# Kernel optimization log

Hardware: AMD Instinct MI355X
Metric: run time of the kernel (lower is better)

The kernel has to match this reference:

```python
import jax, jax.numpy as jnp
import numpy as np

NUM_LEVELS = 16
LEVEL_DIM = 2
BASE_RES = 16
MAX_RES = 2048
HASHMAP_SIZE = 1 << 19
N_POINTS = 2000000

# Instant-NGP geometric progression of grid resolutions
_scale = np.exp2(np.log2(MAX_RES / BASE_RES) / (NUM_LEVELS - 1))
RESOLUTIONS = [int(np.ceil(BASE_RES * _scale ** l)) for l in range(NUM_LEVELS)]

# corner offsets of the unit cube, shape [8, 3]
_OFFS = np.stack(np.meshgrid([0, 1], [0, 1], [0, 1], indexing='ij'), -1).reshape(8, 3)
_PRIMES = np.array([1, 2654435761, 805459861], dtype=np.uint32)


def grid_encode(x, table):
    """x: [N,3] in [0,1]; table: [L, T, F] -> [N, L*F]."""
    offs = jnp.asarray(_OFFS, dtype=jnp.int32)          # [8,3]
    feats = []
    for l, res in enumerate(RESOLUTIONS):
        pos = x * (res - 1)                              # [N,3]
        pos_i = jnp.clip(jnp.floor(pos).astype(jnp.int32), 0, res - 2)
        frac = pos - pos_i.astype(pos.dtype)             # [N,3]
        corners = pos_i[:, None, :] + offs[None]         # [N,8,3]
        if res ** 3 <= HASHMAP_SIZE:
            # dense (collision-free) indexing for coarse levels
            idx = corners[..., 0] + res * (corners[..., 1] + res * corners[..., 2])
        else:
            # spatial hash: xor of coordinate * prime, mod table size
            c = corners.astype(jnp.uint32)
            h = (c[..., 0] * _PRIMES[0]) ^ (c[..., 1] * _PRIMES[1]) ^ (c[..., 2] * _PRIMES[2])
            idx = (h % jnp.uint32(HASHMAP_SIZE)).astype(jnp.int32)
        vals = table[l][idx]                             # [N,8,F] gather
        # multilinear interpolation weights per corner
        w = jnp.prod(jnp.where(offs[None].astype(bool), frac[:, None, :], 1.0 - frac[:, None, :]), axis=-1)  # [N,8]
        feats.append(jnp.einsum('nc,ncf->nf', w, vals))
    return jnp.concatenate(feats, axis=-1)               # [N, 32]


def setup_inputs() -> dict:
    key = jax.random.key(0)
    ks = jax.random.split(key, 6)
    x = jax.random.uniform(ks[0], (N_POINTS, 3), dtype=jnp.float32)
    table = jax.random.uniform(ks[1], (NUM_LEVELS, HASHMAP_SIZE, LEVEL_DIM),
                               dtype=jnp.float32, minval=-1e-4, maxval=1e-4)
    in_dim = NUM_LEVELS * LEVEL_DIM  # 32
    W1 = jax.random.normal(ks[2], (in_dim, 64), dtype=jnp.float32) / np.sqrt(in_dim)
    W2 = jax.random.normal(ks[3], (64, 64), dtype=jnp.float32) / 8.0
    W3 = jax.random.normal(ks[4], (64, 64), dtype=jnp.float32) / 8.0
    Wo = jax.random.normal(ks[5], (64, 1), dtype=jnp.float32) / 8.0
    z = lambda n: jnp.zeros((n,), dtype=jnp.float32)
    return {"x": x, "table": table, "W1": W1, "b1": z(64), "W2": W2, "b2": z(64),
            "W3": W3, "b3": z(64), "Wo": Wo, "bo": z(1)}


def reference(x, table, W1, b1, W2, b2, W3, b3, Wo, bo):
    h = grid_encode(x, table)                 # [N,32]
    h = jax.nn.relu(h @ W1 + b1)
    h = jax.nn.relu(h @ W2 + b2)
    h = jax.nn.relu(h @ W3 + b3)
    return h @ Wo + bo                        # [N,1]
```

## Files before the change

### kernel.cpp

```cpp
#include <hip/hip_runtime.h>
#include <hip/hip_fp16.h>
#include <cmath>
#include <cstdint>


#define HASH_SZ (1u << 19)
#define HMASK   (HASH_SZ - 1u)
#define PR2 2654435761u
#define PR3 805459861u

typedef float v2f __attribute__((ext_vector_type(2)));
typedef float v4f __attribute__((ext_vector_type(4)));
typedef v4f v4fu __attribute__((aligned(8)));
typedef v2f v2fu __attribute__((aligned(8)));
typedef short bf16x8 __attribute__((ext_vector_type(8)));
typedef float f32x4 __attribute__((ext_vector_type(4)));
typedef unsigned int u32;
typedef u32 u32x2 __attribute__((ext_vector_type(2)));
typedef u32 u32x4 __attribute__((ext_vector_type(4)));
typedef u32x4 u32x4u __attribute__((aligned(8)));

struct ResArr { int r[16]; };

__device__ __forceinline__ unsigned short bf16_rne(float f) {
    union { float f; unsigned u; } v; v.f = f;
    unsigned u = v.u;
    unsigned r = (u + 0x7fffu + ((u >> 16) & 1u)) >> 16;
    return (unsigned short)r;
}
__device__ __forceinline__ float bf16f(unsigned short h) {
    union { unsigned u; float f; } v; v.u = ((unsigned)h) << 16;
    return v.f;
}
__device__ __forceinline__ void split8(const float* x, bf16x8& hi, bf16x8& lo) {
    #pragma unroll
    for (int j = 0; j < 8; ++j) {
        union { float f; unsigned u; } v; v.f = x[j];
        const unsigned hu = v.u & 0xffff0000u;
        hi[j] = (short)(hu >> 16);
        union { unsigned u; float f; } hf; hf.u = hu;
        const float d = x[j] - hf.f;
        union { float f; unsigned u; } dv; dv.f = d;
        lo[j] = (short)((dv.u + 0x7fffu + ((dv.u >> 16) & 1u)) >> 16);
    }
}
__device__ __forceinline__ u32 rne16u(float f) {
    union { float f; u32 u; } v; v.f = f;
    return (v.u + 0x7fffu + ((v.u >> 16) & 1u)) >> 16;
}
__device__ __forceinline__ u32x2 pack_split2(float f0, float f1) {
    union { float f; u32 u; } a, b; a.f = f0; b.f = f1;
    const u32 h0 = a.u & 0xffff0000u, h1 = b.u & 0xffff0000u;
    union { u32 u; float f; } ha, hb; ha.u = h0; hb.u = h1;
    u32x2 r;
    r.x = (h0 >> 16) | h1;
    r.y = rne16u(f0 - ha.f) | (rne16u(f1 - hb.f) << 16);
    return r;
}

__device__ __forceinline__ u32 pkh(float f0, float f1) {
    const __half h0 = __float2half_rn(f0), h1 = __float2half_rn(f1);
    return (u32)__half_as_ushort(h0) | ((u32)__half_as_ushort(h1) << 16);
}
__device__ __forceinline__ v2f cvt2(u32 e) {
    __half2 h;
    *reinterpret_cast<u32*>(&h) = e;
    v2f r; r.x = __low2float(h); r.y = __high2float(h);
    return r;
}
__device__ __forceinline__ u32 sel4(u32x4 P, u32 k) {
    const u32 a = (k & 1u) ? P.y : P.x;
    const u32 b = (k & 1u) ? P.w : P.z;
    return (k & 2u) ? b : a;
}

__global__ __launch_bounds__(256, 8)
void cvt_table(const float* __restrict__ table, u32* __restrict__ tab16, int total)
{
    const int e0 = (blockIdx.x * 256 + threadIdx.x) * 4;
    if (e0 >= total) return;
    const v4f a = __builtin_nontemporal_load((const v4f*)(table + 2 * (size_t)e0));
    const v4f b = __builtin_nontemporal_load((const v4f*)(table + 2 * (size_t)e0 + 4));
    u32x4 o;
    o.x = pkh(a.x, a.y); o.y = pkh(a.z, a.w);
    o.z = pkh(b.x, b.y); o.w = pkh(b.z, b.w);
    *(u32x4*)(tab16 + e0) = o;
}

__device__ __forceinline__ void gather16_one(
    const u32* __restrict__ tab, int res, bool dense,
    float px, float py, float pz, float& A0, float& A1)
{
    const float rf = (float)(res - 1);
    const float fx = px * rf, fy = py * rf, fz = pz * rf;
    int ix = (int)floorf(fx), iy = (int)floorf(fy), iz = (int)floorf(fz);
    ix = min(max(ix, 0), res - 2);
    iy = min(max(iy, 0), res - 2);
    iz = min(max(iz, 0), res - 2);
    const float tx = fx - (float)ix, ty = fy - (float)iy, tz = fz - (float)iz;
    const float sx = 1.f - tx, sy = 1.f - ty, sz = 1.f - tz;
    float a0 = 0.f, a1 = 0.f;

    if (dense) {
        const int b0 = ix + res * (iy + res * iz);
        #pragma unroll
        for (int c = 0; c < 4; ++c) {
            const int dy = c >> 1, dz = c & 1;
            const u32 idx0 = (u32)(b0 + res * dy + res * res * dz);
            const u32x4u Pv = *(const u32x4u*)(tab + (idx0 & ~1u));
            const bool hi = (idx0 & 1u) != 0u;
            const u32 e0 = hi ? Pv.y : Pv.x;
            const u32 e1 = hi ? Pv.z : Pv.y;
            const float wyz = (dy ? ty : sy) * (dz ? tz : sz);
            const float w0 = sx * wyz, w1 = tx * wyz;
            const v2f f0 = cvt2(e0), f1 = cvt2(e1);
            a0 = fmaf(w0, f0.x, a0); a1 = fmaf(w0, f0.y, a1);
            a0 = fmaf(w1, f1.x, a0); a1 = fmaf(w1, f1.y, a1);
        }
    } else {
        u32 i1a[4], k0[4];
        u32x4 P[4];
        #pragma unroll
        for (int c = 0; c < 4; ++c) {
            const int dy = c >> 1, dz = c & 1;
            const u32 r = (u32)(iy + dy) * PR2 ^ (u32)(iz + dz) * PR3;
            const u32 i0 = ((u32)ix ^ r) & HMASK;
            i1a[c] = ((u32)(ix + 1) ^ r) & HMASK;
            k0[c] = i0 & 3u;
            P[c] = *(const u32x4*)(tab + (i0 & ~3u));
        }
        const bool extra = ((ix & 3) == 3);
        u32 O[4];
        if (extra) {
            #pragma unroll
            for (int c = 0; c < 4; ++c) O[c] = tab[i1a[c]];
        } else {
            #pragma unroll
            for (int c = 0; c < 4; ++c) O[c] = 0u;
        }
        #pragma unroll
        for (int c = 0; c < 4; ++c) {
            const int dy = c >> 1, dz = c & 1;
            const u32 e0 = sel4(P[c], k0[c]);
            const u32 e1w = sel4(P[c], i1a[c] & 3u);
            const u32 e1 = extra ? O[c] : e1w;
            const float wyz = (dy ? ty : sy) * (dz ? tz : sz);
            const float w0 = sx * wyz, w1 = tx * wyz;
            const v2f f0 = cvt2(e0), f1 = cvt2(e1);
            a0 = fmaf(w0, f0.x, a0); a1 = fmaf(w0, f0.y, a1);
            a0 = fmaf(w1, f1.x, a0); a1 = fmaf(w1, f1.y, a1);
        }
    }
    A0 = a0; A1 = a1;
}

__global__ void prep_weights(const float* __restrict__ W1,
                             const float* __restrict__ W2,
                             const float* __restrict__ W3,
                             unsigned short* __restrict__ wb)
{
    const int tid = threadIdx.x;
    const int nb = tid >> 6, lane = tid & 63;
    const int l15 = lane & 15, q = lane >> 4;
    #pragma unroll
    for (int j = 0; j < 8; ++j) {
        const float v = W1[(q * 8 + j) * 64 + nb * 16 + l15];
        const unsigned short h = bf16_rne(v);
        wb[(nb * 64 + lane) * 8 + j] = h;
        wb[2048 + (nb * 64 + lane) * 8 + j] = bf16_rne(v - bf16f(h));
    }
    #pragma unroll
    for (int kb = 0; kb < 2; ++kb) {
        #pragma unroll
        for (int j = 0; j < 8; ++j) {
            const int row = kb * 32 + q * 8 + j;
            const int idx = ((kb * 4 + nb) * 64 + lane) * 8 + j;
            float v = W2[row * 64 + nb * 16 + l15];
            unsigned short h = bf16_rne(v);
            wb[4096 + idx] = h;
            wb[8192 + idx] = bf16_rne(v - bf16f(h));
            v = W3[row * 64 + nb * 16 + l15];
            h = bf16_rne(v);
            wb[12288 + idx] = h;
            wb[16384 + idx] = bf16_rne(v - bf16f(h));
        }
    }
}

__device__ __forceinline__ void mlp_block(
    const u32x2* __restrict__ featT,
    const unsigned short* __restrict__ wb,
    const float* __restrict__ b1, const float* __restrict__ b2,
    const float* __restrict__ b3,
    const float* __restrict__ Wo, const float* __restrict__ bo,
    float* __restrict__ out, int n, int ns, int mb)
{
    const int wave = threadIdx.x >> 6;
    const int lane = threadIdx.x & 63;
    const int l15 = lane & 15, quad = lane >> 4;
    const int p0 = (mb * 4 + wave) * 32;
    if (p0 >= n) return;

    bf16x8 bh[2], bl[2];
    #pragma unroll
    for (int t = 0; t < 2; ++t) {
        const int p = p0 + t * 16 + l15;
        const int pl = (p < n) ? p : (n - 1);
        u32x4 hw, lw;
        #pragma unroll
        for (int jj = 0; jj < 4; ++jj) {
            const u32x2 v = featT[(size_t)(quad * 4 + jj) * ns + pl];
            hw[jj] = v.x; lw[jj] = v.y;
        }
        bh[t] = *(bf16x8*)&hw;
        bl[t] = *(bf16x8*)&lw;
    }

    f32x4 acc[2][4];
    #pragma unroll
    for (int nb = 0; nb < 4; ++nb) {
        const bf16x8 wh = *(const bf16x8*)(wb + (nb * 64 + lane) * 8);
        const bf16x8 wl = *(const bf16x8*)(wb + 2048 + (nb * 64 + lane) * 8);
        const f32x4 bv = *(const f32x4*)(b1 + nb * 16 + quad * 4);
        #pragma unroll
        for (int t = 0; t < 2; ++t) {
            f32x4 c = bv;
            c = __builtin_amdgcn_mfma_f32_16x16x32_bf16(wh, bl[t], c, 0, 0, 0);
            c = __builtin_amdgcn_mfma_f32_16x16x32_bf16(wl, bh[t], c, 0, 0, 0);
            c = __builtin_amdgcn_mfma_f32_16x16x32_bf16(wh, bh[t], c, 0, 0, 0);
            acc[t][nb] = c;
        }
    }

    #pragma unroll
    for (int layer = 0; layer < 2; ++layer) {
        bf16x8 nh[2][2], nl[2][2];
        #pragma unroll
        for (int t = 0; t < 2; ++t) {
            #pragma unroll
            for (int kb = 0; kb < 2; ++kb) {
                float v[8];
                #pragma unroll
                for (int rr = 0; rr < 4; ++rr) {
                    float xq = fmaxf(acc[t][2 * kb][rr],     0.f);
                    float yq = fmaxf(acc[t][2 * kb + 1][rr], 0.f);
                    asm("v_permlane32_swap_b32 %0, %1" : "+v"(xq), "+v"(yq));
                    asm("v_permlane16_swap_b32 %0, %1" : "+v"(xq), "+v"(yq));
                    v[rr]     = xq;
                    v[4 + rr] = yq;
                }
                split8(v, nh[t][kb], nl[t][kb]);
            }
        }
        const int base_h = layer ? 12288 : 4096;
        const int base_l = layer ? 16384 : 8192;
        const float* __restrict__ bias = layer ? b3 : b2;
        #pragma unroll
        for (int nb = 0; nb < 4; ++nb) {
            const f32x4 bv = *(const f32x4*)(bias + nb * 16 + quad * 4);
            f32x4 c[2];
            #pragma unroll
            for (int t = 0; t < 2; ++t) c[t] = bv;
            #pragma unroll
            for (int kb = 0; kb < 2; ++kb) {
                const int idx = ((kb * 4 + nb) * 64 + lane) * 8;
                const bf16x8 wh = *(const bf16x8*)(wb + base_h + idx);
                const bf16x8 wl = *(const bf16x8*)(wb + base_l + idx);
                #pragma unroll
                for (int t = 0; t < 2; ++t) {
                    c[t] = __builtin_amdgcn_mfma_f32_16x16x32_bf16(wh, nl[t][kb], c[t], 0, 0, 0);
                    c[t] = __builtin_amdgcn_mfma_f32_16x16x32_bf16(wl, nh[t][kb], c[t], 0, 0, 0);
                    c[t] = __builtin_amdgcn_mfma_f32_16x16x32_bf16(wh, nh[t][kb], c[t], 0, 0, 0);
                }
            }
            #pragma unroll
            for (int t = 0; t < 2; ++t) acc[t][nb] = c[t];
        }
    }

    float part[2];
    #pragma unroll
    for (int t = 0; t < 2; ++t) {
        float s = 0.f;
        #pragma unroll
        for (int nb = 0; nb < 4; ++nb) {
            const f32x4 wo4 = *(const f32x4*)(Wo + nb * 16 + quad * 4);
            #pragma unroll
            for (int r = 0; r < 4; ++r)
                s = fmaf(fmaxf(acc[t][nb][r], 0.f), wo4[r], s);
        }
        part[t] = s;
    }
    #pragma unroll
    for (int t = 0; t < 2; ++t) {
        part[t] += __shfl_xor(part[t], 16, 64);
        part[t] += __shfl_xor(part[t], 32, 64);
    }
    if (quad == 0) {
        const float b = bo[0];
        #pragma unroll
        for (int t = 0; t < 2; ++t) {
            const int po = p0 + t * 16 + l15;
            if (po < n) out[po] = part[t] + b;
        }
    }
}

__global__ __launch_bounds__(256, 4)
void mlp_mfma(const u32x2* __restrict__ featT,
              const unsigned short* __restrict__ wb,
              const float* __restrict__ b1, const float* __restrict__ b2,
              const float* __restrict__ b3,
              const float* __restrict__ Wo, const float* __restrict__ bo,
              float* __restrict__ out, int n, int ns)
{
    mlp_block(featT, wb, b1, b2, b3, Wo, bo, out, n, ns, blockIdx.x);
}

__global__ __launch_bounds__(256, 4)
void fused_q(const float* __restrict__ xe, const u32* __restrict__ tab16,
             u32x2* __restrict__ fe, int ne, int nse,
             const u32x2* __restrict__ fm,
             const unsigned short* __restrict__ wb,
             const float* __restrict__ b1, const float* __restrict__ b2,
             const float* __restrict__ b3,
             const float* __restrict__ Wo, const float* __restrict__ bo,
             float* __restrict__ outm, int nm, int nsm,
             ResArr rv, int de, int bpl, int M, int ilv)
{
    const int b = blockIdx.x;
    int eb;
    if (ilv) {
        const int q4 = b >> 2, r4 = b & 3;
        if (r4 == 3 && q4 < M) {
            mlp_block(fm, wb, b1, b2, b3, Wo, bo, outm, nm, nsm, q4);
            return;
        }
        eb = b - ((r4 == 3) ? M : min(q4, M));
    } else {
        if (b < M) {
            mlp_block(fm, wb, b1, b2, b3, Wo, bo, outm, nm, nsm, b);
            return;
        }
        eb = b - M;
    }
    const int lvl = eb / bpl;
    if (lvl >= 16) return;
    const int lblk = eb - lvl * bpl;
    const int res = rv.r[lvl];
    const bool dense = (lvl < de);
    const u32* tbl = tab16 + (size_t)lvl * HASH_SZ;

    const int nth2 = bpl * 512;
    for (int q = (lblk * 256 + (int)threadIdx.x) * 2; q < ne; q += nth2) {
        float p0x, p0y, p0z, p1x, p1y, p1z;
        const bool two = (q + 1 < ne);
        if (two) {
            const v4fu a = __builtin_nontemporal_load((const v4fu*)(xe + 3 * q));
            const v2f  bb = __builtin_nontemporal_load((const v2fu*)(xe + 3 * q + 4));
            p0x = a.x; p0y = a.y; p0z = a.z; p1x = a.w; p1y = bb.x; p1z = bb.y;
        } else {
            p0x = xe[3 * q]; p0y = xe[3 * q + 1]; p0z = xe[3 * q + 2];
            p1x = p0x; p1y = p0y; p1z = p0z;
        }
        float a00, a01, a10, a11;
        gather16_one(tbl, res, dense, p0x, p0y, p0z, a00, a01);
        gather16_one(tbl, res, dense, p1x, p1y, p1z, a10, a11);
        if (two) {
            const u32x2 e0 = pack_split2(a00, a01);
            const u32x2 e1 = pack_split2(a10, a11);
            u32x4 st; st.x = e0.x; st.y = e0.y; st.z = e1.x; st.w = e1.y;
            __builtin_nontemporal_store(st, (u32x4*)&fe[(size_t)lvl * nse + q]);
        } else {
            __builtin_nontemporal_store(pack_split2(a00, a01),
                                        &fe[(size_t)lvl * nse + q]);
        }
    }
}

__device__ __forceinline__ void gather_one(
    const v2f* __restrict__ tbl, int res, bool dense,
    float px, float py, float pz, float& A0, float& A1)
{
    const float rf = (float)(res - 1);
    const float fx = px * rf, fy = py * rf, fz = pz * rf;
    int ix = (int)floorf(fx), iy = (int)floorf(fy), iz = (int)floorf(fz);
    ix = min(max(ix, 0), res - 2);
    iy = min(max(iy, 0), res - 2);
    iz = min(max(iz, 0), res - 2);
    const float tx = fx - (float)ix, ty = fy - (float)iy, tz = fz - (float)iz;
    const float sx = 1.f - tx, sy = 1.f - ty, sz = 1.f - tz;
    float a0 = 0.f, a1 = 0.f;

    if (dense) {
        const int b0 = ix + res * (iy + res * iz);
        v4fu P[4];
        #pragma unroll
        for (int c = 0; c < 4; ++c) {
            const int dy = c >> 1, dz = c & 1;
            P[c] = *(const v4fu*)((const float*)tbl + 2 * (b0 + res * dy + res * res * dz));
        }
        #pragma unroll
        for (int c = 0; c < 4; ++c) {
            const int dy = c >> 1, dz = c & 1;
            const float wyz = (dy ? ty : sy) * (dz ? tz : sz);
            const float w0 = sx * wyz, w1 = tx * wyz;
            a0 = fmaf(w0, P[c].x, a0); a1 = fmaf(w0, P[c].y, a1);
            a0 = fmaf(w1, P[c].z, a0); a1 = fmaf(w1, P[c].w, a1);
        }
    } else {
        uint32_t i0[4], i1[4];
        v4f P[4];
        #pragma unroll
        for (int c = 0; c < 4; ++c) {
            const int dy = c >> 1, dz = c & 1;
            const uint32_t r = (uint32_t)(iy + dy) * PR2 ^ (uint32_t)(iz + dz) * PR3;
            i0[c] = ((uint32_t)ix ^ r) & HMASK;
            i1[c] = ((uint32_t)(ix + 1) ^ r) & HMASK;
            P[c] = *(const v4f*)((const float*)tbl + 2 * (i0[c] & ~1u));
        }
        const bool odd = (ix & 1);
        v2f O[4];
        if (odd) {
            #pragma unroll
            for (int c = 0; c < 4; ++c) O[c] = tbl[i1[c]];
        } else {
            #pragma unroll
            for (int c = 0; c < 4; ++c) { v2f z = {0.f, 0.f}; O[c] = z; }
        }
        #pragma unroll
        for (int c = 0; c < 4; ++c) {
            const int dy = c >> 1, dz = c & 1;
            const bool hi = (i0[c] & 1);
            v2f c0, e;
            c0.x = hi ? P[c].z : P[c].x;  c0.y = hi ? P[c].w : P[c].y;
            e.x  = hi ? P[c].x : P[c].z;  e.y  = hi ? P[c].y : P[c].w;
            const v2f c1 = odd ? O[c] : e;
            const float wyz = (dy ? ty : sy) * (dz ? tz : sz);
            const float w0 = sx * wyz, w1 = tx * wyz;
            a0 = fmaf(w0, c0.x, a0); a1 = fmaf(w0, c0.y, a1);
            a0 = fmaf(w1, c1.x, a0); a1 = fmaf(w1, c1.y, a1);
        }
    }
    A0 = a0; A1 = a1;
}

template<int NLEV>
__global__ __launch_bounds__(256, 8)
void encode_k(const float* __restrict__ x, const float* __restrict__ table,
              u32x2* __restrict__ featT, int n, int lb, ResArr rv)
{
    const int nth2 = gridDim.x * 512;
    for (int q = (blockIdx.x * 256 + threadIdx.x) * 2; q < n; q += nth2) {
        float p0x, p0y, p0z, p1x, p1y, p1z;
        const bool two = (q + 1 < n);
        if (two) {
            const v4fu a = __builtin_nontemporal_load((const v4fu*)(x + 3 * q));
            const v2f  b = __builtin_nontemporal_load((const v2fu*)(x + 3 * q + 4));
            p0x = a.x; p0y = a.y; p0z = a.z; p1x = a.w; p1y = b.x; p1z = b.y;
        } else {
            p0x = x[3 * q]; p0y = x[3 * q + 1]; p0z = x[3 * q + 2];
            p1x = p0x; p1y = p0y; p1z = p0z;
        }
        #pragma unroll
        for (int il = 0; il < NLEV; ++il) {
            const int l = lb + il;
            const int res = rv.r[l];
            const bool dense = ((long long)res * res * res <= (long long)HASH_SZ);
            const v2f* tbl = (const v2f*)table + (size_t)l * HASH_SZ;
            float a00, a01, a10, a11;
            gather_one(tbl, res, dense, p0x, p0y, p0z, a00, a01);
            gather_one(tbl, res, dense, p1x, p1y, p1z, a10, a11);
            if (two) {
                const u32x2 e0 = pack_split2(a00, a01);
                const u32x2 e1 = pack_split2(a10, a11);
                u32x4 st; st.x = e0.x; st.y = e0.y; st.z = e1.x; st.w = e1.y;
                __builtin_nontemporal_store(st, (u32x4*)&featT[(size_t)l * n + q]);
            } else {
                __builtin_nontemporal_store(pack_split2(a00, a01),
                                            &featT[(size_t)l * n + q]);
            }
        }
    }
}

__global__ __launch_bounds__(256, 3)
void mlp_forward(const u32x2* __restrict__ featT,
                 const float* __restrict__ W1, const float* __restrict__ b1,
                 const float* __restrict__ W2, const float* __restrict__ b2,
                 const float* __restrict__ W3, const float* __restrict__ b3,
                 const float* __restrict__ Wo, const float* __restrict__ bo,
                 float* __restrict__ out, int n)
{
    const int p = blockIdx.x * 256 + threadIdx.x;
    if (p >= n) return;
    const v2f z2 = {0.f, 0.f};
    v2f A[32], B[32];
    #pragma unroll
    for (int jq = 0; jq < 16; ++jq) {
        const v4f b = *(const v4f*)(b1 + 4 * jq);
        A[2 * jq] = b.xy; A[2 * jq + 1] = b.zw;
    }
    #pragma unroll
    for (int l = 0; l < 16; ++l) {
        const u32x2 e = __builtin_nontemporal_load(&featT[(size_t)l * n + p]);
        union { u32 u; float f; } h0, h1, l0, l1;
        h0.u = e.x << 16; h1.u = e.x & 0xffff0000u;
        l0.u = e.y << 16; l1.u = e.y & 0xffff0000u;
        v2f f; f.x = h0.f + l0.f; f.y = h1.f + l1.f;
        const v4f* w0 = (const v4f*)(W1 + (size_t)(2 * l) * 64);
        const v4f* w1 = (const v4f*)(W1 + (size_t)(2 * l + 1) * 64);
        const v2f hh0 = {f.x, f.x}, hh1 = {f.y, f.y};
        #pragma unroll
        for (int jq = 0; jq < 16; ++jq) {
            const v4f wa = w0[jq];
            A[2 * jq]     = __builtin_elementwise_fma(hh0, wa.xy, A[2 * jq]);
            A[2 * jq + 1] = __builtin_elementwise_fma(hh0, wa.zw, A[2 * jq + 1]);
        }
        #pragma unroll
        for (int jq = 0; jq < 16; ++jq) {
            const v4f wb2 = w1[jq];
            A[2 * jq]     = __builtin_elementwise_fma(hh1, wb2.xy, A[2 * jq]);
            A[2 * jq + 1] = __builtin_elementwise_fma(hh1, wb2.zw, A[2 * jq + 1]);
        }
    }
    #pragma unroll
    for (int j = 0; j < 32; ++j) A[j] = __builtin_elementwise_max(A[j], z2);
    #pragma unroll
    for (int jq = 0; jq < 16; ++jq) {
        const v4f b = *(const v4f*)(b2 + 4 * jq);
        B[2 * jq] = b.xy; B[2 * jq + 1] = b.zw;
    }
    #pragma unroll
    for (int k = 0; k < 64; ++k) {
        const float hv = A[k >> 1][k & 1];
        const v2f h = {hv, hv};
        const v4f* w = (const v4f*)(W2 + (size_t)k * 64);
        #pragma unroll
        for (int jq = 0; jq < 16; ++jq) {
            const v4f wa = w[jq];
            B[2 * jq]     = __builtin_elementwise_fma(h, wa.xy, B[2 * jq]);
            B[2 * jq + 1] = __builtin_elementwise_fma(h, wa.zw, B[2 * jq + 1]);
        }
    }
    #pragma unroll
    for (int j = 0; j < 32; ++j) B[j] = __builtin_elementwise_max(B[j], z2);
    #pragma unroll
    for (int jq = 0; jq < 16; ++jq) {
        const v4f b = *(const v4f*)(b3 + 4 * jq);
        A[2 * jq] = b.xy; A[2 * jq + 1] = b.zw;
    }
    #pragma unroll
    for (int k = 0; k < 64; ++k) {
        const float hv = B[k >> 1][k & 1];
        const v2f h = {hv, hv};
        const v4f* w = (const v4f*)(W3 + (size_t)k * 64);
        #pragma unroll
        for (int jq = 0; jq < 16; ++jq) {
            const v4f wa = w[jq];
            A[2 * jq]     = __builtin_elementwise_fma(h, wa.xy, A[2 * jq]);
            A[2 * jq + 1] = __builtin_elementwise_fma(h, wa.zw, A[2 * jq + 1]);
        }
    }
    v2f o2 = z2;
    #pragma unroll
    for (int jq = 0; jq < 16; ++jq) {
        const v4f wa = *(const v4f*)(Wo + 4 * jq);
        o2 = __builtin_elementwise_fma(__builtin_elementwise_max(A[2 * jq], z2),     wa.xy, o2);
        o2 = __builtin_elementwise_fma(__builtin_elementwise_max(A[2 * jq + 1], z2), wa.zw, o2);
    }
    out[p] = o2.x + o2.y + bo[0];
}

__global__ __launch_bounds__(256, 2)
void hashpinn_fused(const float* __restrict__ x,
                    const float* __restrict__ table,
                    const float* __restrict__ W1, const float* __restrict__ b1,
                    const float* __restrict__ W2, const float* __restrict__ b2,
                    const float* __restrict__ W3, const float* __restrict__ b3,
                    const float* __restrict__ Wo, const float* __restrict__ bo,
                    float* __restrict__ out, int n, ResArr rv)
{
    const int p = blockIdx.x * 256 + threadIdx.x;
    if (p >= n) return;
    const float px = x[3*p+0], py = x[3*p+1], pz = x[3*p+2];
    float feat[32];
    #pragma unroll
    for (int l = 0; l < 16; ++l) {
        const int res = rv.r[l];
        const float rf = (float)(res - 1);
        const float fx = px*rf, fy = py*rf, fz = pz*rf;
        int ix=(int)floorf(fx), iy=(int)floorf(fy), iz=(int)floorf(fz);
        ix=min(max(ix,0),res-2); iy=min(max(iy,0),res-2); iz=min(max(iz,0),res-2);
        const float tx=fx-(float)ix, ty=fy-(float)iy, tz=fz-(float)iz;
        const float sx=1.f-tx, sy=1.f-ty, sz=1.f-tz;
        const float2* tbl=(const float2*)table+(size_t)l*HASH_SZ;
        const bool dense=((long long)res*res*res<=(long long)HASH_SZ);
        float a0=0.f, a1=0.f;
        #pragma unroll
        for (int c=0;c<8;++c){
            const uint32_t cx=(uint32_t)(ix+((c>>2)&1));
            const uint32_t cy=(uint32_t)(iy+((c>>1)&1));
            const uint32_t cz=(uint32_t)(iz+(c&1));
            uint32_t idx = dense ? cx+(uint32_t)res*(cy+(uint32_t)res*cz)
                                 : ((cx*1u ^ cy*PR2 ^ cz*PR3)&HMASK);
            const float2 v=tbl[idx];
            const float w=(((c>>2)&1)?tx:sx)*(((c>>1)&1)?ty:sy)*((c&1)?tz:sz);
            a0=fmaf(w,v.x,a0); a1=fmaf(w,v.y,a1);
        }
        feat[2*l]=a0; feat[2*l+1]=a1;
    }
    float A[64], B[64];
    #pragma unroll
    for (int j=0;j<64;++j) A[j]=b1[j];
    #pragma unroll
    for (int k=0;k<32;++k){ const float h=feat[k];
        #pragma unroll
        for (int j=0;j<64;++j) A[j]=fmaf(h,W1[k*64+j],A[j]); }
    #pragma unroll 1
    for (int it=0;it<2;++it){
        const float* W = it?W3:W2; const float* bb = it?b3:b2;
        #pragma unroll
        for (int j=0;j<64;++j){ A[j]=fmaxf(A[j],0.f); B[j]=bb[j]; }
        #pragma unroll
        for (int k=0;k<64;++k){ const float h=A[k];
            #pragma unroll
            for (int j=0;j<64;++j) B[j]=fmaf(h,W[k*64+j],B[j]); }
        #pragma unroll
        for (int j=0;j<64;++j) A[j]=B[j];
    }
    float o=bo[0];
    #pragma unroll
    for (int j=0;j<64;++j) o=fmaf(fmaxf(A[j],0.f),Wo[j],o);
    out[p]=o;
}

static inline void launch_encode(int nlev, const float* x, const float* table,
                                 u32x2* featT, int n, int lb, const ResArr& rv,
                                 hipStream_t stream) {
    const dim3 g(4096), b(256);
    switch (nlev) {
        case 1: hipLaunchKernelGGL(encode_k<1>, g, b, 0, stream, x, table, featT, n, lb, rv); break;
        case 2: hipLaunchKernelGGL(encode_k<2>, g, b, 0, stream, x, table, featT, n, lb, rv); break;
        case 3: hipLaunchKernelGGL(encode_k<3>, g, b, 0, stream, x, table, featT, n, lb, rv); break;
        case 4: hipLaunchKernelGGL(encode_k<4>, g, b, 0, stream, x, table, featT, n, lb, rv); break;
        case 5: hipLaunchKernelGGL(encode_k<5>, g, b, 0, stream, x, table, featT, n, lb, rv); break;
        case 6: hipLaunchKernelGGL(encode_k<6>, g, b, 0, stream, x, table, featT, n, lb, rv); break;
        case 7: hipLaunchKernelGGL(encode_k<7>, g, b, 0, stream, x, table, featT, n, lb, rv); break;
        default: hipLaunchKernelGGL(encode_k<8>, g, b, 0, stream, x, table, featT, n, lb, rv); break;
    }
}

extern "C" void kernel_launch(void* const* d_in, const int* in_sizes, int n_in,
                              void* d_out, int out_size, void* d_ws, size_t ws_size,
                              hipStream_t stream) {
    const float* x     = (const float*)d_in[0];
    const float* table = (const float*)d_in[1];
    const float* W1    = (const float*)d_in[2];
    const float* b1    = (const float*)d_in[3];
    const float* W2    = (const float*)d_in[4];
    const float* b2    = (const float*)d_in[5];
    const float* W3    = (const float*)d_in[6];
    const float* b3    = (const float*)d_in[7];
    const float* Wo    = (const float*)d_in[8];
    const float* bo    = (const float*)d_in[9];
    float* out = (float*)d_out;

    const int n = in_sizes[0] / 3;

    ResArr rv;
    const double scale = std::exp2(std::log2(2048.0 / 16.0) / 15.0);
    for (int l = 0; l < 16; ++l)
        rv.r[l] = (int)std::ceil(16.0 * std::pow(scale, (double)l));

    int dense_end = 0;
    while (dense_end < 16) {
        long long r = rv.r[dense_end];
        if (r * r * r <= (long long)HASH_SZ) ++dense_end; else break;
    }
    if (dense_end > 8) dense_end = 8;

    const size_t wb_bytes = 20480 * sizeof(unsigned short);
    const size_t tab16_bytes = (size_t)16 * HASH_SZ * sizeof(u32);
    const int total_entries = 16 * (int)HASH_SZ;

    const int Q = 4;
    int qoff[Q + 1];
    {
        int base = ((n + Q - 1) / Q + 1) & ~1;
        for (int i = 0; i <= Q; ++i) {
            long long o = (long long)base * i;
            qoff[i] = (int)(o < n ? o : n);
        }
        qoff[Q] = n;
    }
    int nsmax = 2;
    for (int i = 0; i < Q; ++i) {
        const int nq = qoff[i + 1] - qoff[i];
        const int ns = (nq + 1) & ~1;
        if (ns > nsmax) nsmax = ns;
    }
    const size_t slab_bytes = (size_t)nsmax * 16 * sizeof(u32x2);
    const size_t feat_bytes = (size_t)n * 16 * sizeof(u32x2);

    if (ws_size >= 2 * slab_bytes + wb_bytes + tab16_bytes) {
        u32x2* fA = (u32x2*)d_ws;
        u32x2* fB = (u32x2*)((char*)d_ws + slab_bytes);
        unsigned short* wb = (unsigned short*)((char*)d_ws + 2 * slab_bytes);
        u32* tab16 = (u32*)((char*)d_ws + 2 * slab_bytes + wb_bytes);

        hipLaunchKernelGGL(prep_weights, dim3(1), dim3(256), 0, stream, W1, W2, W3, wb);
        hipLaunchKernelGGL(cvt_table, dim3(8192), dim3(256), 0, stream,
                           table, tab16, total_entries);

        int prev_n = 0, prev_ns = 0, prev_off = 0;
        for (int i = 0; i < Q; ++i) {
            const int nq = qoff[i + 1] - qoff[i];
            const int ns = (nq + 1) & ~1;
            u32x2* cur = (i & 1) ? fB : fA;
            u32x2* prv = (i & 1) ? fA : fB;
            const int M = prev_n > 0 ? (prev_n + 127) / 128 : 0;
            if (nq <= 0) {
                if (M > 0)
                    hipLaunchKernelGGL(mlp_mfma, dim3(M), dim3(256), 0, stream,
                                       prv, wb, b1, b2, b3, Wo, bo,
                                       out + prev_off, prev_n, prev_ns);
                prev_n = 0;
                continue;
            }
            const int bpl = (nq + 511) / 512;
            const int T = 16 * bpl + M;
            const int ilv = (M > 0 && 4 * M <= T) ? 1 : 0;
            hipLaunchKernelGGL(fused_q, dim3(T), dim3(256), 0, stream,
                               x + (size_t)3 * qoff[i], tab16, cur, nq, ns,
                               prv, wb, b1, b2, b3, Wo, bo,
                               out + prev_off, prev_n, prev_ns,
                               rv, dense_end, bpl, M, ilv);
            prev_n = nq; prev_ns = ns; prev_off = qoff[i];
        }
        if (prev_n > 0) {
            u32x2* last = ((Q - 1) & 1) ? fB : fA;
            const int M = (prev_n + 127) / 128;
            hipLaunchKernelGGL(mlp_mfma, dim3(M), dim3(256), 0, stream,
                               last, wb, b1, b2, b3, Wo, bo,
                               out + prev_off, prev_n, prev_ns);
        }
    } else if (ws_size >= feat_bytes + wb_bytes) {
        u32x2* featT = (u32x2*)d_ws;
        unsigned short* wb = (unsigned short*)((char*)d_ws + feat_bytes);

        hipLaunchKernelGGL(prep_weights, dim3(1), dim3(256), 0, stream, W1, W2, W3, wb);

        if (dense_end > 0)
            launch_encode(dense_end, x, table, featT, n, 0, rv, stream);
        for (int l = dense_end; l < 16; ++l)
            launch_encode(1, x, table, featT, n, l, rv, stream);

        const int nblocks = (n + 127) / 128;
        hipLaunchKernelGGL(mlp_mfma, dim3(nblocks), dim3(256), 0, stream,
                           featT, wb, b1, b2, b3, Wo, bo, out, n, n);
    } else if (ws_size >= feat_bytes) {
        u32x2* featT = (u32x2*)d_ws;
        if (dense_end > 0)
            launch_encode(dense_end, x, table, featT, n, 0, rv, stream);
        for (int l = dense_end; l < 16; ++l)
            launch_encode(1, x, table, featT, n, l, rv, stream);
        hipLaunchKernelGGL(mlp_forward, dim3((n + 255) / 256), dim3(256), 0, stream,
                           featT, W1, b1, W2, b2, W3, b3, Wo, bo, out, n);
    } else {
        hipLaunchKernelGGL(hashpinn_fused, dim3((n + 255) / 256), dim3(256), 0, stream,
                           x, table, W1, b1, W2, b2, W3, b3, Wo, bo, out, n, rv);
    }
}
```

Baseline: 966.6 us.

## Spread MLP blocks evenly among encode blocks and add nontemporal feature loads

The fixed 1-in-4 interleave of MLP blocks within the fused encode+MLP grid becomes a uniform stride K = T/M, so the previous chunk's MLP work is spread across the whole grid instead of bunched at the front. Feature reads and output writes in the MLP now use nontemporal hints, which should keep them from evicting hash-table lines from cache. Launch bounds on the fused kernel go from 4 to 8 waves-per-EU blocks, which may force register spilling in the large encode path.

```diff
diff --git a/kernel.cpp b/kernel.cpp
--- a/kernel.cpp
+++ b/kernel.cpp
@@ -209,7 +209,8 @@
         u32x4 hw, lw;
         #pragma unroll
         for (int jj = 0; jj < 4; ++jj) {
-            const u32x2 v = featT[(size_t)(quad * 4 + jj) * ns + pl];
+            const u32x2 v = __builtin_nontemporal_load(
+                &featT[(size_t)(quad * 4 + jj) * ns + pl]);
             hw[jj] = v.x; lw[jj] = v.y;
         }
         bh[t] = *(bf16x8*)&hw;
@@ -301,7 +302,7 @@
         #pragma unroll
         for (int t = 0; t < 2; ++t) {
             const int po = p0 + t * 16 + l15;
-            if (po < n) out[po] = part[t] + b;
+            if (po < n) __builtin_nontemporal_store(part[t] + b, &out[po]);
         }
     }
 }
@@ -317,7 +318,7 @@
     mlp_block(featT, wb, b1, b2, b3, Wo, bo, out, n, ns, blockIdx.x);
 }
 
-__global__ __launch_bounds__(256, 4)
+__global__ __launch_bounds__(256, 8)
 void fused_q(const float* __restrict__ xe, const u32* __restrict__ tab16,
              u32x2* __restrict__ fe, int ne, int nse,
              const u32x2* __restrict__ fm,
@@ -326,24 +327,15 @@
              const float* __restrict__ b3,
              const float* __restrict__ Wo, const float* __restrict__ bo,
              float* __restrict__ outm, int nm, int nsm,
-             ResArr rv, int de, int bpl, int M, int ilv)
+             ResArr rv, int de, int bpl, int M, int K)
 {
     const int b = blockIdx.x;
-    int eb;
-    if (ilv) {
-        const int q4 = b >> 2, r4 = b & 3;
-        if (r4 == 3 && q4 < M) {
-            mlp_block(fm, wb, b1, b2, b3, Wo, bo, outm, nm, nsm, q4);
-            return;
-        }
-        eb = b - ((r4 == 3) ? M : min(q4, M));
-    } else {
-        if (b < M) {
-            mlp_block(fm, wb, b1, b2, b3, Wo, bo, outm, nm, nsm, b);
-            return;
-        }
-        eb = b - M;
-    }
+    const int qk = b / K, rk = b - qk * K;
+    if (rk == K - 1 && qk < M) {
+        mlp_block(fm, wb, b1, b2, b3, Wo, bo, outm, nm, nsm, qk);
+        return;
+    }
+    const int eb = b - min(qk, M);
     const int lvl = eb / bpl;
     if (lvl >= 16) return;
     const int lblk = eb - lvl * bpl;
@@ -730,12 +722,18 @@
             }
             const int bpl = (nq + 511) / 512;
             const int T = 16 * bpl + M;
-            const int ilv = (M > 0 && 4 * M <= T) ? 1 : 0;
+            int K;
+            if (M > 0) {
+                K = T / M;
+                if (K < 2) K = 2;
+            } else {
+                K = 0x40000000;
+            }
             hipLaunchKernelGGL(fused_q, dim3(T), dim3(256), 0, stream,
                                x + (size_t)3 * qoff[i], tab16, cur, nq, ns,
                                prv, wb, b1, b2, b3, Wo, bo,
                                out + prev_off, prev_n, prev_ns,
-                               rv, dense_end, bpl, M, ilv);
+                               rv, dense_end, bpl, M, K);
             prev_n = nq; prev_ns = ns; prev_off = qoff[i];
         }
         if (prev_n > 0) {
```

Result: slower. 1.138 ms (+17.7%).
